# Performance work log

Hardware: AMD Instinct MI355X
Metric: run time of the kernel (lower is better)

Reference implementation:

```python
import jax, jax.numpy as jnp
import numpy as np

T, E = 8192, 1024
LAYER_DEPTH, NUM_LAYERS = 12, 24


def _init_params():
    ratio_0_to_1 = LAYER_DEPTH / (NUM_LAYERS - 1)
    ratio_1_to_almost_0 = 1.0 - LAYER_DEPTH / NUM_LAYERS
    zigzag = 0.5 * (jnp.arange(1, E + 1) % 3 - 1)
    time_first = jnp.full(E, jnp.log(0.3), dtype=jnp.float32) + zigzag.astype(jnp.float32)
    h = jnp.arange(0, E, dtype=jnp.float32)
    time_decay = (-5 + 8 * (h / (E - 1)) ** (0.7 + 1.3 * ratio_0_to_1)).astype(jnp.float32)
    xr = jnp.arange(E, dtype=jnp.float32) / E
    time_mix_k = jnp.power(xr, ratio_1_to_almost_0)
    time_mix_v = time_mix_k + 0.3 * ratio_0_to_1
    time_mix_r = jnp.power(xr, 0.5 * ratio_1_to_almost_0)
    return time_first, time_decay, time_mix_k, time_mix_v, time_mix_r


def setup_inputs() -> dict:
    key = jax.random.key(0)
    kx, kk_, kv_, kr_, ko_ = jax.random.split(key, 5)
    scale = 1.0 / np.sqrt(E)
    tf, td, tmk, tmv, tmr = _init_params()
    return {
        "x": jax.random.normal(kx, (T, E), dtype=jnp.float32),
        "sx": jnp.zeros((E,), jnp.float32),
        "aa": jnp.zeros((E,), jnp.float32),
        "bb": jnp.zeros((E,), jnp.float32),
        "pp": jnp.zeros((E,), jnp.float32),
        "time_first": tf,
        "time_decay": td,
        "time_mix_k": tmk,
        "time_mix_v": tmv,
        "time_mix_r": tmr,
        "Wk": jax.random.normal(kk_, (E, E), jnp.float32) * scale,
        "Wv": jax.random.normal(kv_, (E, E), jnp.float32) * scale,
        "Wr": jax.random.normal(kr_, (E, E), jnp.float32) * scale,
        "Wo": jax.random.normal(ko_, (E, E), jnp.float32) * scale,
    }


def reference(x, sx, aa, bb, pp, time_first, time_decay,
              time_mix_k, time_mix_v, time_mix_r, Wk, Wv, Wr, Wo):
    # token-shift: previous token (or carried state sx at t=0)  [T, E]
    sx_seq = jnp.concatenate((sx[None, :], x[:-1, :]), axis=0)
    kx = x * time_mix_k + sx_seq * (1.0 - time_mix_k)
    vx = x * time_mix_v + sx_seq * (1.0 - time_mix_v)
    rx = x * time_mix_r + sx_seq * (1.0 - time_mix_r)

    r = jax.nn.sigmoid(rx @ Wr)  # [T, E]
    k = kx @ Wk                  # [T, E]
    v = vx @ Wv                  # [T, E]
    decay = -jnp.exp(time_decay)  # [E]

    def step(state, kv):
        aa_, bb_, pp_ = state
        kk, vv = kv
        ww = time_first + kk
        p = jnp.maximum(pp_, ww)
        e1 = jnp.exp(pp_ - p)
        e2 = jnp.exp(ww - p)
        out = (e1 * aa_ + e2 * vv) / (e1 * bb_ + e2)
        ww2 = decay + pp_
        p2 = jnp.maximum(ww2, kk)
        e1b = jnp.exp(ww2 - p2)
        e2b = jnp.exp(kk - p2)
        return (e1b * aa_ + e2b * vv, e1b * bb_ + e2b, p2), out

    (aa_f, bb_f, pp_f), wkv = jax.lax.scan(step, (aa, bb, pp), (k, v))
    out = x + (r * wkv) @ Wo
    return out, x[-1, :], aa_f, bb_f, pp_f
```

## Files before the change

### kernel.cpp

```cpp
#include <hip/hip_runtime.h>
#include <cstdint>
#include <cstddef>

typedef __bf16 bf16x8 __attribute__((ext_vector_type(8)));
typedef float  f32x4  __attribute__((ext_vector_type(4)));

#define TT 8192
#define EE 1024
#define LDSK 40

__device__ __forceinline__ unsigned short f2bf(float f) {
    union { float f; unsigned int u; } v; v.f = f;
    unsigned int r = v.u + 0x7FFFu + ((v.u >> 16) & 1u);
    return (unsigned short)(r >> 16);
}
__device__ __forceinline__ float b2f(unsigned int h) {
    union { unsigned int u; float f; } v; v.u = h << 16; return v.f;
}
__device__ __forceinline__ void gload_lds16(const void* g, void* l) {
    __builtin_amdgcn_global_load_lds((__attribute__((address_space(1))) void*)g,
                                     (__attribute__((address_space(3))) void*)l, 16, 0, 0);
}

__global__ void wt_kernel(const float* __restrict__ Wk, const float* __restrict__ Wv,
                          const float* __restrict__ Wr, const float* __restrict__ Wo,
                          unsigned short* __restrict__ Tk, unsigned short* __restrict__ Tv,
                          unsigned short* __restrict__ Tr, unsigned short* __restrict__ To) {
    __shared__ float tile[32][33];
    const float* W; unsigned short* D;
    switch (blockIdx.z) {
        case 0:  W = Wk; D = Tk; break;
        case 1:  W = Wv; D = Tv; break;
        case 2:  W = Wr; D = Tr; break;
        default: W = Wo; D = To; break;
    }
    const int bx = blockIdx.x * 32, by = blockIdx.y * 32;
    const int tx = threadIdx.x, ty = threadIdx.y;
#pragma unroll
    for (int r = 0; r < 4; ++r)
        tile[ty + 8 * r][tx] = W[(size_t)(by + ty + 8 * r) * EE + bx + tx];
    __syncthreads();
#pragma unroll
    for (int r = 0; r < 4; ++r)
        D[(size_t)(bx + ty + 8 * r) * EE + by + tx] = f2bf(tile[tx][ty + 8 * r]);
}

__global__ void prep_kernel(const float* __restrict__ Wk, const float* __restrict__ Wv,
                            const float* __restrict__ Wr, const float* __restrict__ Wo,
                            unsigned short* __restrict__ Tk, unsigned short* __restrict__ Tv,
                            unsigned short* __restrict__ Tr, unsigned short* __restrict__ To,
                            const float* __restrict__ x, const float* __restrict__ sx,
                            const float* __restrict__ tmk, const float* __restrict__ tmv,
                            const float* __restrict__ tmr,
                            unsigned short* __restrict__ kxb, unsigned short* __restrict__ vxb,
                            unsigned short* __restrict__ rxb) {
    const int bid = blockIdx.x;
    if (bid < 4096) {
        __shared__ float tile[32][33];
        const int z = bid >> 10;
        const float* W; unsigned short* D;
        switch (z) {
            case 0:  W = Wk; D = Tk; break;
            case 1:  W = Wv; D = Tv; break;
            case 2:  W = Wr; D = Tr; break;
            default: W = Wo; D = To; break;
        }
        const int by = ((bid >> 5) & 31) * 32, bx = (bid & 31) * 32;
        const int tx = threadIdx.x & 31, ty = threadIdx.x >> 5;
#pragma unroll
        for (int r = 0; r < 4; ++r)
            tile[ty + 8 * r][tx] = W[(size_t)(by + ty + 8 * r) * EE + bx + tx];
        __syncthreads();
#pragma unroll
        for (int r = 0; r < 4; ++r)
            D[(size_t)(bx + ty + 8 * r) * EE + by + tx] = f2bf(tile[tx][ty + 8 * r]);
    } else {
        const int gid  = (bid - 4096) * 256 + threadIdx.x;
        const int base = gid * 4;
        const int t = base >> 10;
        const int e = base & (EE - 1);
        float4 xv = *(const float4*)(x + base);
        float4 pv = (t > 0) ? *(const float4*)(x + base - EE) : *(const float4*)(sx + e);
        float4 mk = *(const float4*)(tmk + e);
        float4 mv = *(const float4*)(tmv + e);
        float4 mr = *(const float4*)(tmr + e);
        ushort4 ko, vo, ro;
        ko.x = f2bf(fmaf(mk.x, xv.x - pv.x, pv.x));
        ko.y = f2bf(fmaf(mk.y, xv.y - pv.y, pv.y));
        ko.z = f2bf(fmaf(mk.z, xv.z - pv.z, pv.z));
        ko.w = f2bf(fmaf(mk.w, xv.w - pv.w, pv.w));
        vo.x = f2bf(fmaf(mv.x, xv.x - pv.x, pv.x));
        vo.y = f2bf(fmaf(mv.y, xv.y - pv.y, pv.y));
        vo.z = f2bf(fmaf(mv.z, xv.z - pv.z, pv.z));
        vo.w = f2bf(fmaf(mv.w, xv.w - pv.w, pv.w));
        ro.x = f2bf(fmaf(mr.x, xv.x - pv.x, pv.x));
        ro.y = f2bf(fmaf(mr.y, xv.y - pv.y, pv.y));
        ro.z = f2bf(fmaf(mr.z, xv.z - pv.z, pv.z));
        ro.w = f2bf(fmaf(mr.w, xv.w - pv.w, pv.w));
        *(ushort4*)(kxb + base) = ko;
        *(ushort4*)(vxb + base) = vo;
        *(ushort4*)(rxb + base) = ro;
    }
}

__global__ __launch_bounds__(256, 4) void gemm_kvr3(
        const unsigned short* __restrict__ kxb, const unsigned short* __restrict__ vxb,
        const unsigned short* __restrict__ rxb,
        const unsigned short* __restrict__ Wkt, const unsigned short* __restrict__ Wvt,
        const unsigned short* __restrict__ Wrt,
        unsigned short* __restrict__ kf, unsigned short* __restrict__ vf,
        unsigned short* __restrict__ ry) {
    __shared__ __align__(16) unsigned short As[128 * 64];
    __shared__ __align__(16) unsigned short Bs[128 * 64];
    const int z = blockIdx.z;
    const unsigned short* A  = (z == 0) ? kxb : (z == 1) ? vxb : rxb;
    const unsigned short* Bt = (z == 0) ? Wkt : (z == 1) ? Wvt : Wrt;
    unsigned short* C        = (z == 0) ? kf  : (z == 1) ? vf  : ry;

    const int tid  = threadIdx.x;
    const int wave = tid >> 6, lane = tid & 63;
    const int wm = (wave >> 1) * 64, wn = (wave & 1) * 64;
    const int l15 = lane & 15, lq = lane >> 4;
    const int lrow = lane >> 3;
    const int lcolg = (((lane & 7) ^ lrow) & 7) * 8;
    const int sw = l15 & 7;
    const int bm = blockIdx.x * 128, bn = blockIdx.y * 128;

    f32x4 acc[4][4] = {};

    for (int kt = 0; kt < 1024; kt += 64) {
        __syncthreads();
#pragma unroll
        for (int p = 0; p < 4; ++p) {
            const int r0 = p * 32 + wave * 8;
            gload_lds16(A  + (size_t)(bm + r0 + lrow) * 1024 + kt + lcolg, &As[r0 * 64]);
            gload_lds16(Bt + (size_t)(bn + r0 + lrow) * 1024 + kt + lcolg, &Bs[r0 * 64]);
        }
        __syncthreads();
#pragma unroll
        for (int h = 0; h < 2; ++h) {
            bf16x8 af[4], bfr[4];
#pragma unroll
            for (int i = 0; i < 4; ++i) {
                const int g = ((h * 4 + lq) ^ sw) * 8;
                af[i]  = *(const bf16x8*)(&As[(wm + i * 16 + l15) * 64 + g]);
                bfr[i] = *(const bf16x8*)(&Bs[(wn + i * 16 + l15) * 64 + g]);
            }
#pragma unroll
            for (int i = 0; i < 4; ++i)
#pragma unroll
                for (int j = 0; j < 4; ++j)
                    acc[i][j] = __builtin_amdgcn_mfma_f32_16x16x32_bf16(af[i], bfr[j], acc[i][j], 0, 0, 0);
        }
    }

    const bool sig = (z == 2);
#pragma unroll
    for (int i = 0; i < 4; ++i)
#pragma unroll
        for (int j = 0; j < 4; ++j) {
            const int col = bn + wn + j * 16 + l15;
#pragma unroll
            for (int r = 0; r < 4; ++r) {
                const int row = bm + wm + i * 16 + lq * 4 + r;
                float val = acc[i][j][r];
                if (sig) val = 1.f / (1.f + __expf(-val));
                C[(size_t)row * 1024 + col] = f2bf(val);
            }
        }
}

__global__ __launch_bounds__(256, 4) void gemm_wo(const unsigned short* __restrict__ A,
                                                  const unsigned short* __restrict__ Bt,
                                                  const float* __restrict__ Res,
                                                  float* __restrict__ C) {
    __shared__ __align__(16) unsigned short As[128 * 64];
    __shared__ __align__(16) unsigned short Bs[128 * 64];
    const int tid  = threadIdx.x;
    const int wave = tid >> 6, lane = tid & 63;
    const int wm = (wave >> 1) * 64, wn = (wave & 1) * 64;
    const int l15 = lane & 15, lq = lane >> 4;
    const int lrow = lane >> 3;
    const int lcolg = (((lane & 7) ^ lrow) & 7) * 8;
    const int sw = l15 & 7;
    const int bm = blockIdx.x * 128, bn = blockIdx.y * 128;

    f32x4 acc[4][4] = {};

    for (int kt = 0; kt < 1024; kt += 64) {
        __syncthreads();
#pragma unroll
        for (int p = 0; p < 4; ++p) {
            const int r0 = p * 32 + wave * 8;
            gload_lds16(A  + (size_t)(bm + r0 + lrow) * 1024 + kt + lcolg, &As[r0 * 64]);
            gload_lds16(Bt + (size_t)(bn + r0 + lrow) * 1024 + kt + lcolg, &Bs[r0 * 64]);
        }
        __syncthreads();
#pragma unroll
        for (int h = 0; h < 2; ++h) {
            bf16x8 af[4], bfr[4];
#pragma unroll
            for (int i = 0; i < 4; ++i) {
                const int g = ((h * 4 + lq) ^ sw) * 8;
                af[i]  = *(const bf16x8*)(&As[(wm + i * 16 + l15) * 64 + g]);
                bfr[i] = *(const bf16x8*)(&Bs[(wn + i * 16 + l15) * 64 + g]);
            }
#pragma unroll
            for (int i = 0; i < 4; ++i)
#pragma unroll
                for (int j = 0; j < 4; ++j)
                    acc[i][j] = __builtin_amdgcn_mfma_f32_16x16x32_bf16(af[i], bfr[j], acc[i][j], 0, 0, 0);
        }
    }

#pragma unroll
    for (int i = 0; i < 4; ++i)
#pragma unroll
        for (int j = 0; j < 4; ++j) {
            const int col = bn + wn + j * 16 + l15;
#pragma unroll
            for (int r = 0; r < 4; ++r) {
                const int row = bm + wm + i * 16 + lq * 4 + r;
                const size_t idx = (size_t)row * 1024 + col;
                C[idx] = acc[i][j][r] + Res[idx];
            }
        }
}

template <int NC>
__global__ void wkv_pass_a(const unsigned short* __restrict__ k,
                           const unsigned short* __restrict__ v,
                           const float* __restrict__ td,
                           float* __restrict__ Sa, float* __restrict__ Sb,
                           float* __restrict__ Sp) {
    const int CL = TT / NC;
    const int gid = blockIdx.x * 256 + threadIdx.x;
    const int c  = gid >> 9;
    const int e0 = (gid & 511) * 2;
    const float2 tdv = *(const float2*)(td + e0);
    float w[2] = { -__expf(tdv.x), -__expf(tdv.y) };
    float sa[2] = {0.f, 0.f}, sb[2] = {0.f, 0.f}, sp[2] = {-1e30f, -1e30f};
    const size_t base = (size_t)c * CL * EE + e0;
#pragma unroll
    for (int i = 0; i < CL; ++i) {
        const unsigned int k2 = *(const unsigned int*)(k + base + (size_t)i * EE);
        const unsigned int v2 = *(const unsigned int*)(v + base + (size_t)i * EE);
        const unsigned short ks[2] = { (unsigned short)(k2 & 0xffffu),
                                       (unsigned short)(k2 >> 16) };
        const unsigned short vs[2] = { (unsigned short)(v2 & 0xffffu),
                                       (unsigned short)(v2 >> 16) };
        const float fi = (float)(CL - 1 - i);
#pragma unroll
        for (int j = 0; j < 2; ++j) {
            const float kk = b2f(ks[j]), vv = b2f(vs[j]);
            const float q  = fmaf(w[j], fi, kk);
            const float p2 = fmaxf(sp[j], q);
            const float e1 = __expf(sp[j] - p2), e2 = __expf(q - p2);
            sa[j] = fmaf(e1, sa[j], e2 * vv);
            sb[j] = fmaf(e1, sb[j], e2);
            sp[j] = p2;
        }
    }
    float2 o;
    o.x = sa[0]; o.y = sa[1]; *(float2*)(Sa + c * EE + e0) = o;
    o.x = sb[0]; o.y = sb[1]; *(float2*)(Sb + c * EE + e0) = o;
    o.x = sp[0]; o.y = sp[1]; *(float2*)(Sp + c * EE + e0) = o;
}

template <int NC>
__global__ void wkv_pass_b_par(const float* __restrict__ aa, const float* __restrict__ bb,
                               const float* __restrict__ pp, const float* __restrict__ td,
                               const float* __restrict__ x,
                               const float* __restrict__ Sa, const float* __restrict__ Sb,
                               const float* __restrict__ Sp,
                               float* __restrict__ ina, float* __restrict__ inb,
                               float* __restrict__ inp, float* __restrict__ outTail) {
    const int CL = TT / NC;
    const int e = blockIdx.x, c = threadIdx.x;
    __shared__ float sA[NC], sB[NC], sP[NC];
    const float w = -__expf(td[e]);

    float a = Sa[c * EE + e], b = Sb[c * EE + e], p = Sp[c * EE + e];

    for (int s = 1; s < NC; s <<= 1) {
        sA[c] = a; sB[c] = b; sP[c] = p;
        __syncthreads();
        if (c >= s) {
            const float myLen = (float)(CL * min(c + 1, s));
            const float aL = sA[c - s], bL = sB[c - s], pL = sP[c - s];
            const float pLd = pL + w * myLen;
            const float pn  = fmaxf(pLd, p);
            const float e1  = __expf(pLd - pn), e2 = __expf(p - pn);
            a = fmaf(e1, aL, e2 * a);
            b = fmaf(e1, bL, e2 * b);
            p = pn;
        }
        __syncthreads();
    }

    sA[c] = a; sB[c] = b; sP[c] = p;
    __syncthreads();

    const float a0 = aa[e], b0 = bb[e], p0 = pp[e];
    float ea, eb, ep;
    if (c == 0) { ea = a0; eb = b0; ep = p0; }
    else {
        const float aL = sA[c - 1], bL = sB[c - 1], pL = sP[c - 1];
        const float p0d = p0 + w * (float)(c * CL);
        const float pn  = fmaxf(p0d, pL);
        const float e1  = __expf(p0d - pn), e2 = __expf(pL - pn);
        ea = fmaf(e1, a0, e2 * aL);
        eb = fmaf(e1, b0, e2 * bL);
        ep = pn;
    }
    ina[e * NC + c] = ea; inb[e * NC + c] = eb; inp[e * NC + c] = ep;

    if (c == NC - 1) {
        const float p0d = p0 + w * (float)TT;
        const float pn  = fmaxf(p0d, p);
        const float e1  = __expf(p0d - pn), e2 = __expf(p - pn);
        outTail[e]          = x[(size_t)(TT - 1) * EE + e];
        outTail[EE + e]     = fmaf(e1, a0, e2 * a);
        outTail[2 * EE + e] = fmaf(e1, b0, e2 * b);
        outTail[3 * EE + e] = pn;
    }
}

template <int NC>
__global__ void wkv_pass_c(const unsigned short* __restrict__ k,
                           const unsigned short* __restrict__ v,
                           const float* __restrict__ tf, const float* __restrict__ td,
                           const float* __restrict__ ina, const float* __restrict__ inb,
                           const float* __restrict__ inp,
                           unsigned short* __restrict__ ry) {
    const int CL = TT / NC;
    const int gid = blockIdx.x * 256 + threadIdx.x;
    const int c  = gid >> 9;
    const int e0 = (gid & 511) * 2;
    const float2 tdv = *(const float2*)(td + e0);
    const float2 tfv = *(const float2*)(tf + e0);
    float w[2] = { -__expf(tdv.x), -__expf(tdv.y) };
    float u[2] = { tfv.x, tfv.y };
    float a[2], b[2], p[2];
#pragma unroll
    for (int j = 0; j < 2; ++j) {
        a[j] = ina[(e0 + j) * NC + c];
        b[j] = inb[(e0 + j) * NC + c];
        p[j] = inp[(e0 + j) * NC + c];
    }
    const size_t base = (size_t)c * CL * EE + e0;
#pragma unroll 4
    for (int i = 0; i < CL; ++i) {
        const size_t idx = base + (size_t)i * EE;
        const unsigned int k2 = *(const unsigned int*)(k + idx);
        const unsigned int v2 = *(const unsigned int*)(v + idx);
        const unsigned int r2 = *(const unsigned int*)(ry + idx);
        const unsigned short ks[2] = { (unsigned short)(k2 & 0xffffu),
                                       (unsigned short)(k2 >> 16) };
        const unsigned short vs[2] = { (unsigned short)(v2 & 0xffffu),
                                       (unsigned short)(v2 >> 16) };
        const unsigned short rs[2] = { (unsigned short)(r2 & 0xffffu),
                                       (unsigned short)(r2 >> 16) };
        unsigned short os[2];
#pragma unroll
        for (int j = 0; j < 2; ++j) {
            const float kk = b2f(ks[j]), vv = b2f(vs[j]), rr = b2f(rs[j]);
            const float ww = u[j] + kk;
            const float pq = fmaxf(p[j], ww);
            const float e1 = __expf(p[j] - pq), e2 = __expf(ww - pq);
            const float wkv = fmaf(e1, a[j], e2 * vv) * __builtin_amdgcn_rcpf(fmaf(e1, b[j], e2));
            os[j] = f2bf(rr * wkv);
            const float ww2 = w[j] + p[j];
            const float p2  = fmaxf(ww2, kk);
            const float e1b = __expf(ww2 - p2), e2b = __expf(kk - p2);
            a[j] = fmaf(e1b, a[j], e2b * vv);
            b[j] = fmaf(e1b, b[j], e2b);
            p[j] = p2;
        }
        *(unsigned int*)(ry + idx) = (unsigned int)os[0] | ((unsigned int)os[1] << 16);
    }
}

__global__ void wkv_pass_b_small(const float* __restrict__ aa, const float* __restrict__ bb,
                                 const float* __restrict__ pp, const float* __restrict__ td,
                                 const float* __restrict__ x,
                                 const float* __restrict__ Sa, const float* __restrict__ Sb,
                                 const float* __restrict__ Sp,
                                 float* __restrict__ ina, float* __restrict__ inb,
                                 float* __restrict__ inp, float* __restrict__ outTail) {
    const int NC = 128, CL = TT / NC;
    const int e = blockIdx.x * 256 + threadIdx.x;
    const float w  = -__expf(td[e]);
    const float wL = w * (float)CL;
    float a = aa[e], b = bb[e], p = pp[e];
    for (int c = 0; c < NC; ++c) {
        ina[e * NC + c] = a; inb[e * NC + c] = b; inp[e * NC + c] = p;
        const int idx = c * EE + e;
        const float sa = Sa[idx], sb = Sb[idx], sp = Sp[idx];
        const float pw = p + wL;
        const float p2 = fmaxf(pw, sp);
        const float e1 = __expf(pw - p2), e2 = __expf(sp - p2);
        a = fmaf(e1, a, e2 * sa);
        b = fmaf(e1, b, e2 * sb);
        p = p2;
    }
    outTail[e]          = x[(size_t)(TT - 1) * EE + e];
    outTail[EE + e]     = a;
    outTail[2 * EE + e] = b;
    outTail[3 * EE + e] = p;
}

__global__ __launch_bounds__(256, 4) void gemm_kvr(
        const float* __restrict__ X, const float* __restrict__ SX,
        const float* __restrict__ tmk, const float* __restrict__ tmv,
        const float* __restrict__ tmr,
        const unsigned short* __restrict__ Wkt, const unsigned short* __restrict__ Wvt,
        const unsigned short* __restrict__ Wrt,
        unsigned short* __restrict__ outK, unsigned short* __restrict__ outV,
        unsigned short* __restrict__ outR) {
    __shared__ __align__(16) unsigned short As[128 * LDSK];
    __shared__ __align__(16) unsigned short Bs[128 * LDSK];
    const int z = blockIdx.z;
    const float* TM = (z == 0) ? tmk : (z == 1) ? tmv : tmr;
    const unsigned short* Bt = (z == 0) ? Wkt : (z == 1) ? Wvt : Wrt;
    unsigned short* Cout = (z == 0) ? outK : (z == 1) ? outV : outR;

    const int tid  = threadIdx.x;
    const int wave = tid >> 6, lane = tid & 63;
    const int wm = (wave >> 1) * 64, wn = (wave & 1) * 64;
    const int l15 = lane & 15, lq = lane >> 4;
    const int bm = blockIdx.x * 128, bn = blockIdx.y * 128;

    f32x4 acc[4][4] = {};

    for (int kt = 0; kt < 1024; kt += 32) {
        __syncthreads();
#pragma unroll
        for (int p = 0; p < 2; ++p) {
            const int li  = p * 256 + tid;
            const int row = li >> 2, q = li & 3;
            const int e0  = kt + q * 8;
            {
                const int t = bm + row;
                const float* xr = X + (size_t)t * EE + e0;
                const float* pr = (t > 0) ? (X + (size_t)(t - 1) * EE + e0) : (SX + e0);
                float4 xa = *(const float4*)xr, xb = *(const float4*)(xr + 4);
                float4 pa = *(const float4*)pr, pb = *(const float4*)(pr + 4);
                float4 ma = *(const float4*)(TM + e0), mb = *(const float4*)(TM + e0 + 4);
                ushort4 lo, hi;
                lo.x = f2bf(fmaf(ma.x, xa.x - pa.x, pa.x));
                lo.y = f2bf(fmaf(ma.y, xa.y - pa.y, pa.y));
                lo.z = f2bf(fmaf(ma.z, xa.z - pa.z, pa.z));
                lo.w = f2bf(fmaf(ma.w, xa.w - pa.w, pa.w));
                hi.x = f2bf(fmaf(mb.x, xb.x - pb.x, pb.x));
                hi.y = f2bf(fmaf(mb.y, xb.y - pb.y, pb.y));
                hi.z = f2bf(fmaf(mb.z, xb.z - pb.z, pb.z));
                hi.w = f2bf(fmaf(mb.w, xb.w - pb.w, pb.w));
                *(ushort4*)(&As[row * LDSK + q * 8])     = lo;
                *(ushort4*)(&As[row * LDSK + q * 8 + 4]) = hi;
            }
            *(uint4*)(&Bs[row * LDSK + q * 8]) =
                *(const uint4*)(Bt + (size_t)(bn + row) * 1024 + e0);
        }
        __syncthreads();
        bf16x8 af[4], bfr[4];
#pragma unroll
        for (int i = 0; i < 4; ++i) {
            af[i]  = *(const bf16x8*)(&As[(wm + i * 16 + l15) * LDSK + lq * 8]);
            bfr[i] = *(const bf16x8*)(&Bs[(wn + i * 16 + l15) * LDSK + lq * 8]);
        }
#pragma unroll
        for (int i = 0; i < 4; ++i)
#pragma unroll
            for (int j = 0; j < 4; ++j)
                acc[i][j] = __builtin_amdgcn_mfma_f32_16x16x32_bf16(af[i], bfr[j], acc[i][j], 0, 0, 0);
    }

    const bool sig = (z == 2);
#pragma unroll
    for (int i = 0; i < 4; ++i)
#pragma unroll
        for (int j = 0; j < 4; ++j) {
            const int col = bn + wn + j * 16 + l15;
#pragma unroll
            for (int r = 0; r < 4; ++r) {
                const int row = bm + wm + i * 16 + lq * 4 + r;
                float val = acc[i][j][r];
                if (sig) val = 1.f / (1.f + __expf(-val));
                Cout[(size_t)row * 1024 + col] = f2bf(val);
            }
        }
}

extern "C" void kernel_launch(void* const* d_in, const int* in_sizes, int n_in,
                              void* d_out, int out_size, void* d_ws, size_t ws_size,
                              hipStream_t stream) {
    const float* x   = (const float*)d_in[0];
    const float* sx  = (const float*)d_in[1];
    const float* aa  = (const float*)d_in[2];
    const float* bb  = (const float*)d_in[3];
    const float* pp  = (const float*)d_in[4];
    const float* tf  = (const float*)d_in[5];
    const float* td  = (const float*)d_in[6];
    const float* tmk = (const float*)d_in[7];
    const float* tmv = (const float*)d_in[8];
    const float* tmr = (const float*)d_in[9];
    const float* Wk  = (const float*)d_in[10];
    const float* Wv  = (const float*)d_in[11];
    const float* Wr  = (const float*)d_in[12];
    const float* Wo  = (const float*)d_in[13];
    float* out = (float*)d_out;

    char* ws = (char*)d_ws;
    const size_t MB = 1ull << 20;

    unsigned short* Wkt = (unsigned short*)(ws + 0 * MB);
    unsigned short* Wvt = (unsigned short*)(ws + 2 * MB);
    unsigned short* Wrt = (unsigned short*)(ws + 4 * MB);
    unsigned short* Wot = (unsigned short*)(ws + 6 * MB);

    if (ws_size >= 75 * MB) {
        unsigned short* rxb = (unsigned short*)(ws + 8 * MB);
        unsigned short* kf  = (unsigned short*)(ws + 24 * MB);
        unsigned short* ry  = (unsigned short*)(ws + 40 * MB);
        unsigned short* vf  = (unsigned short*)(ws + 56 * MB);
        float* Sa  = (float*)(ws + 8  * MB);
        float* Sb  = (float*)(ws + 10 * MB);
        float* Sp  = (float*)(ws + 12 * MB);
        float* ina = (float*)(ws + 14 * MB);
        float* inb = (float*)(ws + 16 * MB);
        float* inp = (float*)(ws + 18 * MB);
        unsigned short* kxb = (unsigned short*)d_out;
        unsigned short* vxb = (unsigned short*)d_out + (size_t)TT * EE;

        prep_kernel<<<12288, 256, 0, stream>>>(Wk, Wv, Wr, Wo, Wkt, Wvt, Wrt, Wot,
                                               x, sx, tmk, tmv, tmr, kxb, vxb, rxb);
        gemm_kvr3<<<dim3(64, 8, 3), 256, 0, stream>>>(kxb, vxb, rxb, Wkt, Wvt, Wrt,
                                                      kf, vf, ry);
        wkv_pass_a<512><<<1024, 256, 0, stream>>>(kf, vf, td, Sa, Sb, Sp);
        wkv_pass_b_par<512><<<EE, 512, 0, stream>>>(aa, bb, pp, td, x, Sa, Sb, Sp,
                                                    ina, inb, inp, out + (size_t)TT * EE);
        wkv_pass_c<512><<<1024, 256, 0, stream>>>(kf, vf, tf, td,
                                                  ina, inb, inp, ry);
        gemm_wo<<<dim3(64, 8), 256, 0, stream>>>(ry, Wot, x, out);
    } else {
        unsigned short* ry = (unsigned short*)(ws + 8 * MB);
        char* scan = ws + 24 * MB;
        const size_t QK = (size_t)128 * EE * sizeof(float);
        float* Sa  = (float*)(scan);
        float* Sb  = (float*)(scan + QK);
        float* Sp  = (float*)(scan + 2 * QK);
        float* ina = (float*)(scan + 3 * QK);
        float* inb = (float*)(scan + 4 * QK);
        float* inp = (float*)(scan + 5 * QK);
        unsigned short* kf = (unsigned short*)d_out;
        unsigned short* vf = (unsigned short*)d_out + (size_t)TT * EE;

        wt_kernel<<<dim3(32, 32, 4), dim3(32, 8), 0, stream>>>(Wk, Wv, Wr, Wo, Wkt, Wvt, Wrt, Wot);
        gemm_kvr<<<dim3(64, 8, 3), 256, 0, stream>>>(x, sx, tmk, tmv, tmr,
                                                     Wkt, Wvt, Wrt, kf, vf, ry);
        wkv_pass_a<128><<<256, 256, 0, stream>>>(kf, vf, td, Sa, Sb, Sp);
        wkv_pass_b_small<<<4, 256, 0, stream>>>(aa, bb, pp, td, x, Sa, Sb, Sp,
                                                ina, inb, inp, out + (size_t)TT * EE);
        wkv_pass_c<128><<<256, 256, 0, stream>>>(kf, vf, tf, td,
                                                 ina, inb, inp, ry);
        gemm_wo<<<dim3(64, 8), 256, 0, stream>>>(ry, Wot, x, out);
    }
}
```

Measured before the change: 242.5 us.

## Fuse three WKV scan passes into one cooperative kernel with grid syncs

Replaces the separate chunk-summary, prefix-combine, and apply kernels of the chunked WKV scan with one cooperative kernel that uses grid-wide syncs between phases. The middle phase now runs 256 threads per channel, each pre-combining two adjacent chunks before a shared-memory prefix scan. The aim is to remove two kernel launches and their inter-kernel gaps. In exchange it relies on all 1024 blocks being co-resident and pays the cost of grid barriers.

After: 629.3 us. 2.6x slower.

```diff
diff --git a/kernel.cpp b/kernel.cpp
--- a/kernel.cpp
+++ b/kernel.cpp
@@ -1,6 +1,9 @@
 #include <hip/hip_runtime.h>
+#include <hip/hip_cooperative_groups.h>
 #include <cstdint>
 #include <cstddef>
+
+namespace cg = cooperative_groups;
 
 typedef __bf16 bf16x8 __attribute__((ext_vector_type(8)));
 typedef float  f32x4  __attribute__((ext_vector_type(4)));
@@ -227,6 +230,187 @@
         }
 }
 
+__global__ __launch_bounds__(256, 4) void wkv_fused3(
+        const unsigned short* __restrict__ kf, const unsigned short* __restrict__ vf,
+        const float* __restrict__ aa, const float* __restrict__ bb,
+        const float* __restrict__ pp, const float* __restrict__ tf,
+        const float* __restrict__ td, const float* __restrict__ x,
+        unsigned short* __restrict__ ry,
+        float* __restrict__ Sa, float* __restrict__ Sb, float* __restrict__ Sp,
+        float* __restrict__ ina, float* __restrict__ inb, float* __restrict__ inp,
+        float* __restrict__ outTail) {
+    const int NC = 512, CL = TT / NC;
+    const int tid = threadIdx.x;
+    __shared__ float sA[256], sB[256], sP[256];
+
+    {
+        const int gid = blockIdx.x * 256 + tid;
+        const int c  = gid >> 9;
+        const int e0 = (gid & 511) * 2;
+        const float2 tdv = *(const float2*)(td + e0);
+        float w[2] = { -__expf(tdv.x), -__expf(tdv.y) };
+        float sa[2] = {0.f, 0.f}, sb[2] = {0.f, 0.f}, sp[2] = {-1e30f, -1e30f};
+        const size_t base = (size_t)c * CL * EE + e0;
+#pragma unroll
+        for (int i = 0; i < CL; ++i) {
+            const unsigned int k2 = *(const unsigned int*)(kf + base + (size_t)i * EE);
+            const unsigned int v2 = *(const unsigned int*)(vf + base + (size_t)i * EE);
+            const unsigned short ks[2] = { (unsigned short)(k2 & 0xffffu),
+                                           (unsigned short)(k2 >> 16) };
+            const unsigned short vs[2] = { (unsigned short)(v2 & 0xffffu),
+                                           (unsigned short)(v2 >> 16) };
+            const float fi = (float)(CL - 1 - i);
+#pragma unroll
+            for (int j = 0; j < 2; ++j) {
+                const float kk = b2f(ks[j]), vv = b2f(vs[j]);
+                const float q  = fmaf(w[j], fi, kk);
+                const float p2 = fmaxf(sp[j], q);
+                const float e1 = __expf(sp[j] - p2), e2 = __expf(q - p2);
+                sa[j] = fmaf(e1, sa[j], e2 * vv);
+                sb[j] = fmaf(e1, sb[j], e2);
+                sp[j] = p2;
+            }
+        }
+        float2 o;
+        o.x = sa[0]; o.y = sa[1]; *(float2*)(Sa + (size_t)c * EE + e0) = o;
+        o.x = sb[0]; o.y = sb[1]; *(float2*)(Sb + (size_t)c * EE + e0) = o;
+        o.x = sp[0]; o.y = sp[1]; *(float2*)(Sp + (size_t)c * EE + e0) = o;
+    }
+    __threadfence();
+    cg::this_grid().sync();
+
+    {
+        const int e = blockIdx.x;
+        const float w = -__expf(td[e]);
+        const float sLa = Sa[(size_t)(2 * tid) * EE + e];
+        const float sLb = Sb[(size_t)(2 * tid) * EE + e];
+        const float sLp = Sp[(size_t)(2 * tid) * EE + e];
+        const float sRa = Sa[(size_t)(2 * tid + 1) * EE + e];
+        const float sRb = Sb[(size_t)(2 * tid + 1) * EE + e];
+        const float sRp = Sp[(size_t)(2 * tid + 1) * EE + e];
+        float Pa, Pb, Pp;
+        {
+            const float pl = sLp + w * (float)CL;
+            const float pn = fmaxf(pl, sRp);
+            const float x1 = __expf(pl - pn), x2 = __expf(sRp - pn);
+            Pa = fmaf(x1, sLa, x2 * sRa);
+            Pb = fmaf(x1, sLb, x2 * sRb);
+            Pp = pn;
+        }
+        for (int s = 1; s < 256; s <<= 1) {
+            sA[tid] = Pa; sB[tid] = Pb; sP[tid] = Pp;
+            __syncthreads();
+            if (tid >= s) {
+                const float pL = sP[tid - s] + w * (float)(CL * 2 * s);
+                const float pn = fmaxf(pL, Pp);
+                const float x1 = __expf(pL - pn), x2 = __expf(Pp - pn);
+                Pa = fmaf(x1, sA[tid - s], x2 * Pa);
+                Pb = fmaf(x1, sB[tid - s], x2 * Pb);
+                Pp = pn;
+            }
+            __syncthreads();
+        }
+        sA[tid] = Pa; sB[tid] = Pb; sP[tid] = Pp;
+        __syncthreads();
+
+        const float a0 = aa[e], b0 = bb[e], p0 = pp[e];
+        {
+            const int cc = 2 * tid;
+            float ea, eb, ep;
+            if (tid == 0) { ea = a0; eb = b0; ep = p0; }
+            else {
+                const float p0d = p0 + w * (float)(cc * CL);
+                const float pn  = fmaxf(p0d, sP[tid - 1]);
+                const float x1  = __expf(p0d - pn), x2 = __expf(sP[tid - 1] - pn);
+                ea = fmaf(x1, a0, x2 * sA[tid - 1]);
+                eb = fmaf(x1, b0, x2 * sB[tid - 1]);
+                ep = pn;
+            }
+            ina[(size_t)e * NC + cc] = ea;
+            inb[(size_t)e * NC + cc] = eb;
+            inp[(size_t)e * NC + cc] = ep;
+        }
+        {
+            float qa, qb, qp;
+            if (tid == 0) { qa = sLa; qb = sLb; qp = sLp; }
+            else {
+                const float pL = sP[tid - 1] + w * (float)CL;
+                const float pn = fmaxf(pL, sLp);
+                const float x1 = __expf(pL - pn), x2 = __expf(sLp - pn);
+                qa = fmaf(x1, sA[tid - 1], x2 * sLa);
+                qb = fmaf(x1, sB[tid - 1], x2 * sLb);
+                qp = pn;
+            }
+            const int cc = 2 * tid + 1;
+            const float p0d = p0 + w * (float)(cc * CL);
+            const float pn  = fmaxf(p0d, qp);
+            const float x1  = __expf(p0d - pn), x2 = __expf(qp - pn);
+            ina[(size_t)e * NC + cc] = fmaf(x1, a0, x2 * qa);
+            inb[(size_t)e * NC + cc] = fmaf(x1, b0, x2 * qb);
+            inp[(size_t)e * NC + cc] = pn;
+        }
+        if (tid == 255) {
+            const float p0d = p0 + w * (float)TT;
+            const float pn  = fmaxf(p0d, Pp);
+            const float x1  = __expf(p0d - pn), x2 = __expf(Pp - pn);
+            outTail[e]          = x[(size_t)(TT - 1) * EE + e];
+            outTail[EE + e]     = fmaf(x1, a0, x2 * Pa);
+            outTail[2 * EE + e] = fmaf(x1, b0, x2 * Pb);
+            outTail[3 * EE + e] = pn;
+        }
+    }
+    __threadfence();
+    cg::this_grid().sync();
+
+    {
+        const int gid = blockIdx.x * 256 + tid;
+        const int c  = gid >> 9;
+        const int e0 = (gid & 511) * 2;
+        const float2 tdv = *(const float2*)(td + e0);
+        const float2 tfv = *(const float2*)(tf + e0);
+        float w[2] = { -__expf(tdv.x), -__expf(tdv.y) };
+        float u[2] = { tfv.x, tfv.y };
+        float a[2], b[2], p[2];
+#pragma unroll
+        for (int j = 0; j < 2; ++j) {
+            a[j] = ina[(size_t)(e0 + j) * NC + c];
+            b[j] = inb[(size_t)(e0 + j) * NC + c];
+            p[j] = inp[(size_t)(e0 + j) * NC + c];
+        }
+        const size_t base = (size_t)c * CL * EE + e0;
+#pragma unroll 4
+        for (int i = 0; i < CL; ++i) {
+            const size_t idx = base + (size_t)i * EE;
+            const unsigned int k2 = *(const unsigned int*)(kf + idx);
+            const unsigned int v2 = *(const unsigned int*)(vf + idx);
+            const unsigned int r2 = *(const unsigned int*)(ry + idx);
+            const unsigned short ks[2] = { (unsigned short)(k2 & 0xffffu),
+                                           (unsigned short)(k2 >> 16) };
+            const unsigned short vs[2] = { (unsigned short)(v2 & 0xffffu),
+                                           (unsigned short)(v2 >> 16) };
+            const unsigned short rs[2] = { (unsigned short)(r2 & 0xffffu),
+                                           (unsigned short)(r2 >> 16) };
+            unsigned short os[2];
+#pragma unroll
+            for (int j = 0; j < 2; ++j) {
+                const float kk = b2f(ks[j]), vv = b2f(vs[j]), rr = b2f(rs[j]);
+                const float ww = u[j] + kk;
+                const float pq = fmaxf(p[j], ww);
+                const float e1 = __expf(p[j] - pq), e2 = __expf(ww - pq);
+                const float wkv = fmaf(e1, a[j], e2 * vv) * __builtin_amdgcn_rcpf(fmaf(e1, b[j], e2));
+                os[j] = f2bf(rr * wkv);
+                const float ww2 = w[j] + p[j];
+                const float p2  = fmaxf(ww2, kk);
+                const float e1b = __expf(ww2 - p2), e2b = __expf(kk - p2);
+                a[j] = fmaf(e1b, a[j], e2b * vv);
+                b[j] = fmaf(e1b, b[j], e2b);
+                p[j] = p2;
+            }
+            *(unsigned int*)(ry + idx) = (unsigned int)os[0] | ((unsigned int)os[1] << 16);
+        }
+    }
+}
+
 template <int NC>
 __global__ void wkv_pass_a(const unsigned short* __restrict__ k,
                            const unsigned short* __restrict__ v,
@@ -265,120 +449,6 @@
     o.x = sa[0]; o.y = sa[1]; *(float2*)(Sa + c * EE + e0) = o;
     o.x = sb[0]; o.y = sb[1]; *(float2*)(Sb + c * EE + e0) = o;
     o.x = sp[0]; o.y = sp[1]; *(float2*)(Sp + c * EE + e0) = o;
-}
-
-template <int NC>
-__global__ void wkv_pass_b_par(const float* __restrict__ aa, const float* __restrict__ bb,
-                               const float* __restrict__ pp, const float* __restrict__ td,
-                               const float* __restrict__ x,
-                               const float* __restrict__ Sa, const float* __restrict__ Sb,
-                               const float* __restrict__ Sp,
-                               float* __restrict__ ina, float* __restrict__ inb,
-                               float* __restrict__ inp, float* __restrict__ outTail) {
-    const int CL = TT / NC;
-    const int e = blockIdx.x, c = threadIdx.x;
-    __shared__ float sA[NC], sB[NC], sP[NC];
-    const float w = -__expf(td[e]);
-
-    float a = Sa[c * EE + e], b = Sb[c * EE + e], p = Sp[c * EE + e];
-
-    for (int s = 1; s < NC; s <<= 1) {
-        sA[c] = a; sB[c] = b; sP[c] = p;
-        __syncthreads();
-        if (c >= s) {
-            const float myLen = (float)(CL * min(c + 1, s));
-            const float aL = sA[c - s], bL = sB[c - s], pL = sP[c - s];
-            const float pLd = pL + w * myLen;
-            const float pn  = fmaxf(pLd, p);
-            const float e1  = __expf(pLd - pn), e2 = __expf(p - pn);
-            a = fmaf(e1, aL, e2 * a);
-            b = fmaf(e1, bL, e2 * b);
-            p = pn;
-        }
-        __syncthreads();
-    }
-
-    sA[c] = a; sB[c] = b; sP[c] = p;
-    __syncthreads();
-
-    const float a0 = aa[e], b0 = bb[e], p0 = pp[e];
-    float ea, eb, ep;
-    if (c == 0) { ea = a0; eb = b0; ep = p0; }
-    else {
-        const float aL = sA[c - 1], bL = sB[c - 1], pL = sP[c - 1];
-        const float p0d = p0 + w * (float)(c * CL);
-        const float pn  = fmaxf(p0d, pL);
-        const float e1  = __expf(p0d - pn), e2 = __expf(pL - pn);
-        ea = fmaf(e1, a0, e2 * aL);
-        eb = fmaf(e1, b0, e2 * bL);
-        ep = pn;
-    }
-    ina[e * NC + c] = ea; inb[e * NC + c] = eb; inp[e * NC + c] = ep;
-
-    if (c == NC - 1) {
-        const float p0d = p0 + w * (float)TT;
-        const float pn  = fmaxf(p0d, p);
-        const float e1  = __expf(p0d - pn), e2 = __expf(p - pn);
-        outTail[e]          = x[(size_t)(TT - 1) * EE + e];
-        outTail[EE + e]     = fmaf(e1, a0, e2 * a);
-        outTail[2 * EE + e] = fmaf(e1, b0, e2 * b);
-        outTail[3 * EE + e] = pn;
-    }
-}
-
-template <int NC>
-__global__ void wkv_pass_c(const unsigned short* __restrict__ k,
-                           const unsigned short* __restrict__ v,
-                           const float* __restrict__ tf, const float* __restrict__ td,
-                           const float* __restrict__ ina, const float* __restrict__ inb,
-                           const float* __restrict__ inp,
-                           unsigned short* __restrict__ ry) {
-    const int CL = TT / NC;
-    const int gid = blockIdx.x * 256 + threadIdx.x;
-    const int c  = gid >> 9;
-    const int e0 = (gid & 511) * 2;
-    const float2 tdv = *(const float2*)(td + e0);
-    const float2 tfv = *(const float2*)(tf + e0);
-    float w[2] = { -__expf(tdv.x), -__expf(tdv.y) };
-    float u[2] = { tfv.x, tfv.y };
-    float a[2], b[2], p[2];
-#pragma unroll
-    for (int j = 0; j < 2; ++j) {
-        a[j] = ina[(e0 + j) * NC + c];
-        b[j] = inb[(e0 + j) * NC + c];
-        p[j] = inp[(e0 + j) * NC + c];
-    }
-    const size_t base = (size_t)c * CL * EE + e0;
-#pragma unroll 4
-    for (int i = 0; i < CL; ++i) {
-        const size_t idx = base + (size_t)i * EE;
-        const unsigned int k2 = *(const unsigned int*)(k + idx);
-        const unsigned int v2 = *(const unsigned int*)(v + idx);
-        const unsigned int r2 = *(const unsigned int*)(ry + idx);
-        const unsigned short ks[2] = { (unsigned short)(k2 & 0xffffu),
-                                       (unsigned short)(k2 >> 16) };
-        const unsigned short vs[2] = { (unsigned short)(v2 & 0xffffu),
-                                       (unsigned short)(v2 >> 16) };
-        const unsigned short rs[2] = { (unsigned short)(r2 & 0xffffu),
-                                       (unsigned short)(r2 >> 16) };
-        unsigned short os[2];
-#pragma unroll
-        for (int j = 0; j < 2; ++j) {
-            const float kk = b2f(ks[j]), vv = b2f(vs[j]), rr = b2f(rs[j]);
-            const float ww = u[j] + kk;
-            const float pq = fmaxf(p[j], ww);
-            const float e1 = __expf(p[j] - pq), e2 = __expf(ww - pq);
-            const float wkv = fmaf(e1, a[j], e2 * vv) * __builtin_amdgcn_rcpf(fmaf(e1, b[j], e2));
-            os[j] = f2bf(rr * wkv);
-            const float ww2 = w[j] + p[j];
-            const float p2  = fmaxf(ww2, kk);
-            const float e1b = __expf(ww2 - p2), e2b = __expf(kk - p2);
-            a[j] = fmaf(e1b, a[j], e2b * vv);
-            b[j] = fmaf(e1b, b[j], e2b);
-            p[j] = p2;
-        }
-        *(unsigned int*)(ry + idx) = (unsigned int)os[0] | ((unsigned int)os[1] << 16);
-    }
 }
 
 __global__ void wkv_pass_b_small(const float* __restrict__ aa, const float* __restrict__ bb,
@@ -410,6 +480,61 @@
     outTail[3 * EE + e] = p;
 }
 
+template <int NC>
+__global__ void wkv_pass_c(const unsigned short* __restrict__ k,
+                           const unsigned short* __restrict__ v,
+                           const float* __restrict__ tf, const float* __restrict__ td,
+                           const float* __restrict__ ina, const float* __restrict__ inb,
+                           const float* __restrict__ inp,
+                           unsigned short* __restrict__ ry) {
+    const int CL = TT / NC;
+    const int gid = blockIdx.x * 256 + threadIdx.x;
+    const int c  = gid >> 9;
+    const int e0 = (gid & 511) * 2;
+    const float2 tdv = *(const float2*)(td + e0);
+    const float2 tfv = *(const float2*)(tf + e0);
+    float w[2] = { -__expf(tdv.x), -__expf(tdv.y) };
+    float u[2] = { tfv.x, tfv.y };
+    float a[2], b[2], p[2];
+#pragma unroll
+    for (int j = 0; j < 2; ++j) {
+        a[j] = ina[(e0 + j) * NC + c];
+        b[j] = inb[(e0 + j) * NC + c];
+        p[j] = inp[(e0 + j) * NC + c];
+    }
+    const size_t base = (size_t)c * CL * EE + e0;
+#pragma unroll 4
+    for (int i = 0; i < CL; ++i) {
+        const size_t idx = base + (size_t)i * EE;
+        const unsigned int k2 = *(const unsigned int*)(k + idx);
+        const unsigned int v2 = *(const unsigned int*)(v + idx);
+        const unsigned int r2 = *(const unsigned int*)(ry + idx);
+        const unsigned short ks[2] = { (unsigned short)(k2 & 0xffffu),
+                                       (unsigned short)(k2 >> 16) };
+        const unsigned short vs[2] = { (unsigned short)(v2 & 0xffffu),
+                                       (unsigned short)(v2 >> 16) };
+        const unsigned short rs[2] = { (unsigned short)(r2 & 0xffffu),
+                                       (unsigned short)(r2 >> 16) };
+        unsigned short os[2];
+#pragma unroll
+        for (int j = 0; j < 2; ++j) {
+            const float kk = b2f(ks[j]), vv = b2f(vs[j]), rr = b2f(rs[j]);
+            const float ww = u[j] + kk;
+            const float pq = fmaxf(p[j], ww);
+            const float e1 = __expf(p[j] - pq), e2 = __expf(ww - pq);
+            const float wkv = fmaf(e1, a[j], e2 * vv) * __builtin_amdgcn_rcpf(fmaf(e1, b[j], e2));
+            os[j] = f2bf(rr * wkv);
+            const float ww2 = w[j] + p[j];
+            const float p2  = fmaxf(ww2, kk);
+            const float e1b = __expf(ww2 - p2), e2b = __expf(kk - p2);
+            a[j] = fmaf(e1b, a[j], e2b * vv);
+            b[j] = fmaf(e1b, b[j], e2b);
+            p[j] = p2;
+        }
+        *(unsigned int*)(ry + idx) = (unsigned int)os[0] | ((unsigned int)os[1] << 16);
+    }
+}
+
 __global__ __launch_bounds__(256, 4) void gemm_kvr(
         const float* __restrict__ X, const float* __restrict__ SX,
         const float* __restrict__ tmk, const float* __restrict__ tmv,
@@ -532,16 +657,24 @@
         float* inp = (float*)(ws + 18 * MB);
         unsigned short* kxb = (unsigned short*)d_out;
         unsigned short* vxb = (unsigned short*)d_out + (size_t)TT * EE;
+        float* outTail = out + (size_t)TT * EE;
 
         prep_kernel<<<12288, 256, 0, stream>>>(Wk, Wv, Wr, Wo, Wkt, Wvt, Wrt, Wot,
                                                x, sx, tmk, tmv, tmr, kxb, vxb, rxb);
         gemm_kvr3<<<dim3(64, 8, 3), 256, 0, stream>>>(kxb, vxb, rxb, Wkt, Wvt, Wrt,
                                                       kf, vf, ry);
-        wkv_pass_a<512><<<1024, 256, 0, stream>>>(kf, vf, td, Sa, Sb, Sp);
-        wkv_pass_b_par<512><<<EE, 512, 0, stream>>>(aa, bb, pp, td, x, Sa, Sb, Sp,
-                                                    ina, inb, inp, out + (size_t)TT * EE);
-        wkv_pass_c<512><<<1024, 256, 0, stream>>>(kf, vf, tf, td,
-                                                  ina, inb, inp, ry);
+        {
+            const unsigned short* kfc = kf;
+            const unsigned short* vfc = vf;
+            void* args[] = {
+                (void*)&kfc, (void*)&vfc, (void*)&aa, (void*)&bb, (void*)&pp,
+                (void*)&tf, (void*)&td, (void*)&x, (void*)&ry,
+                (void*)&Sa, (void*)&Sb, (void*)&Sp,
+                (void*)&ina, (void*)&inb, (void*)&inp, (void*)&outTail
+            };
+            hipLaunchCooperativeKernel((const void*)wkv_fused3, dim3(1024), dim3(256),
+                                       args, 0, stream);
+        }
         gemm_wo<<<dim3(64, 8), 256, 0, stream>>>(ry, Wot, x, out);
     } else {
         unsigned short* ry = (unsigned short*)(ws + 8 * MB);
```
